# Kernel tuning notes

Hardware: AMD Instinct MI355X
Metric: run time of the kernel (lower is better)

Reference implementation:

```python
import jax, jax.numpy as jnp
import numpy as np

VOL = 128
FACTOR = 0.5 * VOL
N = 262144
LAT = 16
B = 8


def setup_inputs() -> dict:
    key = jax.random.key(0)
    ks = jax.random.split(key, 10)
    x = jax.random.normal(ks[0], (B, LAT), jnp.float32)
    inds = jax.random.randint(ks[1], (N, 3), 1, 126, dtype=jnp.int32)
    reference_values = jax.random.normal(ks[2], (N,), jnp.float32)
    # SIREN first layer: U(-1/in, 1/in)
    W0 = jax.random.uniform(ks[3], (LAT, 8), jnp.float32, -1.0 / LAT, 1.0 / LAT)
    b0 = jnp.zeros((8,), jnp.float32)
    # SIREN hidden layers (4 residual layers): U(-sqrt(6/in), sqrt(6/in))
    lim_h = float(np.sqrt(6.0 / 8.0))
    Wh = jax.random.uniform(ks[4], (4, 8, 8), jnp.float32, -lim_h, lim_h)
    bh = jnp.zeros((4, 8), jnp.float32)
    # final glorot-uniform layer: 8 -> 4N
    lim_f = float(np.sqrt(6.0 / (8.0 + 4.0 * N)))
    Wf = jax.random.uniform(ks[5], (8, 4 * N), jnp.float32, -lim_f, lim_f)
    bf = jnp.zeros((4 * N,), jnp.float32)
    return {"x": x, "W0": W0, "b0": b0, "Wh": Wh, "bh": bh, "Wf": Wf,
            "bf": bf, "reference_values": reference_values, "inds": inds}


def _siren_mlp(x, W0, b0, Wh, bh, Wf, bf):
    bf16 = jnp.bfloat16
    h = jnp.sin(30.0 * (x.astype(bf16) @ W0.astype(bf16) + b0.astype(bf16)))
    for i in range(Wh.shape[0]):  # 4 residual sine layers, 8-wide
        h = h + jnp.sin(h @ Wh[i].astype(bf16) + bh[i].astype(bf16))
    return h.astype(jnp.float32) @ Wf + bf  # [B, 4N], final layer in fp32


def reference(x, W0, b0, Wh, bh, Wf, bf, reference_values, inds):
    Bn = x.shape[0]
    out = _siren_mlp(x, W0, b0, Wh, bh, Wf, bf).reshape(Bn, N, 4)
    delta_coords, delta_values = out[..., :3], out[..., 3]
    # coords = stack(z,y,x reversed) normalized to [-1,1)
    coords_norm = (jnp.stack([inds[:, 2], inds[:, 1], inds[:, 0]], axis=1)
                   .astype(jnp.float32) - FACTOR) / FACTOR  # [N,3]
    values = reference_values + delta_values                 # [B,N]
    coords = FACTOR * (coords_norm[None] + delta_coords) + FACTOR  # [B,N,3]
    bposf = jnp.floor(coords)
    bposi = bposf.astype(jnp.int32)
    f = coords - bposf
    fx, fy, fz = f[..., 0], f[..., 1], f[..., 2]
    gx, gy, gz = 1.0 - fx, 1.0 - fy, 1.0 - fz
    # 8 trilinear weights, in the original concat order
    w = jnp.stack([gx * gy * gz, fx * gy * gz, gx * fy * gz, gx * gy * fz,
                   gx * fy * fz, fx * gy * fz, fx * fy * gz, fx * fy * fz],
                  axis=1)                                    # [B,8,N]
    bamp = (values[:, None, :] * w).reshape(Bn, 8 * N)
    offs = jnp.array([[0, 0, 0], [1, 0, 0], [0, 1, 0], [0, 0, 1],
                      [0, 1, 1], [1, 0, 1], [1, 1, 0], [1, 1, 1]], jnp.int32)
    bpos = (bposi[:, None, :, :] + offs[None, :, None, :]).reshape(Bn, 8 * N, 3)

    def scatter(pos, amp):
        return jnp.zeros((VOL, VOL, VOL), jnp.float32).at[
            pos[:, 2], pos[:, 1], pos[:, 0]].add(amp)

    grids = jax.vmap(scatter)(bpos, bamp)  # [B,128,128,128]
    return grids
```

## Files before the change

### kernel.cpp

```cpp
#include <hip/hip_runtime.h>
#include <math.h>

#define VOL   128
#define V2    (VOL*VOL)
#define V3    (VOL*VOL*VOL)
#define NPTS  262144
#define LATD  16
#define BATCH 8
#define FACTORF 64.0f
#define NBINS (VOL*VOL)
#define RZ 8
#define RY 8
#define NREG 256
#define FAR_CAP 8192

#define WS_HBUF    0u
#define WS_HIST    256u
#define WS_START   65792u
#define WS_CURSOR  131584u
#define WS_RANK    197120u
#define WS_KEYS    1245696u
#define WS_FARCNT  2294272u
#define WS_FARLIST 2294528u
#define WS_COORDS  2327296u
#define WS_FULL    35881728u

__device__ __forceinline__ float bf16r(float x) {
    unsigned u = __float_as_uint(x);
    u = (u + 0x7fffu + ((u >> 16) & 1u)) & 0xffff0000u;
    return __uint_as_float(u);
}

__global__ void mlp_kernel(const float* __restrict__ x,
                           const float* __restrict__ W0,
                           const float* __restrict__ b0,
                           const float* __restrict__ Wh,
                           const float* __restrict__ bh,
                           float* __restrict__ hout) {
    int b = threadIdx.x;
    if (b >= BATCH) return;
    float xb[LATD];
    #pragma unroll
    for (int i = 0; i < LATD; ++i) xb[i] = bf16r(x[b*LATD + i]);
    float h[8];
    #pragma unroll
    for (int j = 0; j < 8; ++j) {
        float acc = 0.f;
        #pragma unroll
        for (int i = 0; i < LATD; ++i) acc += xb[i] * bf16r(W0[i*8 + j]);
        float t = bf16r(acc);
        t = bf16r(t + bf16r(b0[j]));
        t = bf16r(30.0f * t);
        h[j] = bf16r(sinf(t));
    }
    for (int l = 0; l < 4; ++l) {
        float nh[8];
        #pragma unroll
        for (int j = 0; j < 8; ++j) {
            float acc = 0.f;
            #pragma unroll
            for (int r = 0; r < 8; ++r) acc += h[r] * bf16r(Wh[(l*8 + r)*8 + j]);
            float t = bf16r(acc);
            t = bf16r(t + bf16r(bh[l*8 + j]));
            float s = bf16r(sinf(t));
            nh[j] = bf16r(h[j] + s);
        }
        #pragma unroll
        for (int j = 0; j < 8; ++j) h[j] = nh[j];
    }
    #pragma unroll
    for (int j = 0; j < 8; ++j) hout[b*8 + j] = h[j];
}

__global__ __launch_bounds__(256) void hist_kernel(const int* __restrict__ inds,
                                                   unsigned* __restrict__ hist) {
    int n = blockIdx.x * 256 + threadIdx.x;
    if (n >= NPTS) return;
    atomicAdd(&hist[inds[n*3]*VOL + inds[n*3+1]], 1u);
}

__global__ __launch_bounds__(256) void scan_kernel(const unsigned* __restrict__ hist,
                                                   unsigned* __restrict__ binstart,
                                                   unsigned* __restrict__ cursor) {
    __shared__ unsigned part[256];
    int t = threadIdx.x;
    const int CH = NBINS / 256;
    unsigned s = 0;
    for (int k = 0; k < CH; ++k) s += hist[t*CH + k];
    part[t] = s; __syncthreads();
    for (int off = 1; off < 256; off <<= 1) {
        unsigned v = (t >= off) ? part[t - off] : 0u;
        __syncthreads();
        part[t] += v;
        __syncthreads();
    }
    unsigned run = (t == 0) ? 0u : part[t - 1];
    for (int k = 0; k < CH; ++k) {
        int idx = t*CH + k;
        binstart[idx] = run;
        cursor[idx]   = run;
        run += hist[idx];
    }
    if (t == 255) binstart[NBINS] = NPTS;
}

__global__ __launch_bounds__(256) void rank_kernel(const int* __restrict__ inds,
                                                   unsigned* __restrict__ cursor,
                                                   unsigned* __restrict__ rank) {
    int n = blockIdx.x * 256 + threadIdx.x;
    if (n >= NPTS) return;
    rank[n] = atomicAdd(&cursor[inds[n*3]*VOL + inds[n*3+1]], 1u);
}

__global__ __launch_bounds__(256) void coords_kernel(
    const float* __restrict__ Wf, const float* __restrict__ bfv_g,
    const float* __restrict__ rv, const int* __restrict__ inds,
    const float* __restrict__ hbuf, const unsigned* __restrict__ rank,
    float4* __restrict__ coords_s, unsigned* __restrict__ keys)
{
    __shared__ float hs[64];
    if (threadIdx.x < 64) hs[threadIdx.x] = hbuf[threadIdx.x];
    __syncthreads();
    int n = blockIdx.x * 256 + threadIdx.x;
    if (n >= NPTS) return;
    int iz = inds[n*3], iy = inds[n*3+1], ix = inds[n*3+2];
    float cnx = ((float)ix - FACTORF) / FACTORF;
    float cny = ((float)iy - FACTORF) / FACTORF;
    float cnz = ((float)iz - FACTORF) / FACTORF;
    float val0 = rv[n];
    float4 bfv = ((const float4*)bfv_g)[n];
    float4 wf[8];
    #pragma unroll
    for (int r = 0; r < 8; ++r)
        wf[r] = ((const float4*)(Wf + (size_t)r * 4 * NPTS))[n];
    unsigned pos = rank[n];
    keys[pos] = (unsigned)((iz << 7) | iy);
    #pragma unroll
    for (int b = 0; b < BATCH; ++b) {
        float o0 = bfv.x, o1 = bfv.y, o2 = bfv.z, o3 = bfv.w;
        #pragma unroll
        for (int r = 0; r < 8; ++r) {
            float hv = hs[b*8 + r];
            o0 = fmaf(hv, wf[r].x, o0);
            o1 = fmaf(hv, wf[r].y, o1);
            o2 = fmaf(hv, wf[r].z, o2);
            o3 = fmaf(hv, wf[r].w, o3);
        }
        float4 c;
        c.x = FACTORF * (cnx + o0) + FACTORF;
        c.y = FACTORF * (cny + o1) + FACTORF;
        c.z = FACTORF * (cnz + o2) + FACTORF;
        c.w = val0 + o3;
        coords_s[(size_t)b * NPTS + pos] = c;
    }
}

__global__ __launch_bounds__(256) void region_kernel(
    const float4* __restrict__ coords_s, const unsigned* __restrict__ keys,
    const unsigned* __restrict__ binstart,
    unsigned* __restrict__ farcnt, unsigned* __restrict__ farlist,
    float* __restrict__ out)
{
    __shared__ float tile[RZ*RY*VOL];
    int tid = threadIdx.x;
    int b   = blockIdx.x >> 8;
    int rid = blockIdx.x & 255;
    int z0 = (rid >> 4) * RZ, y0 = (rid & 15) * RY;
    for (int i = tid; i < RZ*RY*VOL; i += 256) tile[i] = 0.f;
    __syncthreads();

    int ylo = y0 - 3, yhi = y0 + RY + 2;
    int sA0, sA1, sB0, sB1;
    if (ylo < 0)        { sA0 = ylo + VOL; sA1 = VOL; sB0 = 0; sB1 = yhi; }
    else if (yhi > VOL) { sA0 = ylo; sA1 = VOL; sB0 = 0; sB1 = yhi - VOL; }
    else                { sA0 = ylo; sA1 = yhi; sB0 = 0; sB1 = 0; }

    const float4* cb = coords_s + (size_t)b * NPTS;
    const int ox[8] = {0,1,0,0,0,1,1,1};
    const int oy[8] = {0,0,1,0,1,0,1,1};
    const int oz[8] = {0,0,0,1,1,1,0,1};

    for (int zr = z0 - 3; zr < z0 + RZ + 2; ++zr) {
        int zz = (zr + VOL) & (VOL-1);
        int base = zz * VOL;
        for (int sg = 0; sg < 2; ++sg) {
            int a  = sg ? sB0 : sA0;
            int e2 = sg ? sB1 : sA1;
            if (a >= e2) continue;
            unsigned s = binstart[base + a];
            unsigned e = binstart[base + e2];
            for (unsigned i = s + tid; i < e; i += 256) {
                unsigned kv = keys[i];
                int piz = kv >> 7, piy = kv & 127;
                float4 c = cb[i];
                float fxf = floorf(c.x), fyf = floorf(c.y), fzf = floorf(c.z);
                int bx = (int)fxf, by = (int)fyf, bz = (int)fzf;
                bool near = ((unsigned)(bz - piz + 2) <= 4u) &&
                            ((unsigned)(by - piy + 2) <= 4u);
                if (near) {
                    float fx = c.x - fxf, fy = c.y - fyf, fz = c.z - fzf;
                    float gx = 1.f - fx, gy = 1.f - fy, gz = 1.f - fz;
                    float val = c.w;
                    float w[8] = {gx*gy*gz, fx*gy*gz, gx*fy*gz, gx*gy*fz,
                                  gx*fy*fz, fx*gy*fz, fx*fy*gz, fx*fy*fz};
                    #pragma unroll
                    for (int o = 0; o < 8; ++o) {
                        int Z = (bz + oz[o]) & 127;
                        int Y = (by + oy[o]) & 127;
                        int X = (bx + ox[o]) & 127;
                        int dz = Z - z0, dy = Y - y0;
                        if ((unsigned)dz < RZ && (unsigned)dy < RY)
                            atomicAdd(&tile[(dz << 10) + (dy << 7) + X], val * w[o]);
                    }
                } else if (piz >= z0 && piz < z0+RZ && piy >= y0 && piy < y0+RY) {
                    unsigned pos = atomicAdd(farcnt, 1u);
                    if (pos < FAR_CAP) farlist[pos] = (i << 3) | (unsigned)b;
                }
            }
        }
    }
    __syncthreads();
    size_t ob = (size_t)b * V3;
    for (int i = tid; i < RZ*RY*VOL; i += 256) {
        int lz = i >> 10, rem = i & 1023, ly = rem >> 7, lx = rem & 127;
        out[ob + (size_t)(z0+lz)*V2 + (y0+ly)*VOL + lx] = tile[i];
    }
}

__global__ __launch_bounds__(256) void far_kernel(
    const float4* __restrict__ coords_s,
    const unsigned* __restrict__ farcnt, const unsigned* __restrict__ farlist,
    float* __restrict__ out)
{
    unsigned cnt = *farcnt;
    if (cnt > FAR_CAP) cnt = FAR_CAP;
    const int ox[8] = {0,1,0,0,0,1,1,1};
    const int oy[8] = {0,0,1,0,1,0,1,1};
    const int oz[8] = {0,0,0,1,1,1,0,1};
    for (unsigned idx = blockIdx.x * 256 + threadIdx.x; idx < cnt;
         idx += gridDim.x * 256) {
        unsigned e = farlist[idx];
        unsigned pid = e >> 3;
        int b = (int)(e & 7u);
        float4 c = coords_s[(size_t)b * NPTS + pid];
        float fxf = floorf(c.x), fyf = floorf(c.y), fzf = floorf(c.z);
        int bx = (int)fxf, by = (int)fyf, bz = (int)fzf;
        float fx = c.x - fxf, fy = c.y - fyf, fz = c.z - fzf;
        float gx = 1.f - fx, gy = 1.f - fy, gz = 1.f - fz;
        float val = c.w;
        float w[8] = {gx*gy*gz, fx*gy*gz, gx*fy*gz, gx*gy*fz,
                      gx*fy*fz, fx*gy*fz, fx*fy*gz, fx*fy*fz};
        float* ob = out + (size_t)b * V3;
        #pragma unroll
        for (int o = 0; o < 8; ++o) {
            int Z = (bz + oz[o]) & 127;
            int Y = (by + oy[o]) & 127;
            int X = (bx + ox[o]) & 127;
            atomicAdd(ob + (size_t)Z*V2 + Y*VOL + X, val * w[o]);
        }
    }
}

__global__ __launch_bounds__(256) void scatter_fallback(
    const float* __restrict__ Wf, const float* __restrict__ bfv_g,
    const float* __restrict__ rv, const int* __restrict__ inds,
    const float* __restrict__ hbuf, float* __restrict__ out)
{
    __shared__ float hs[BATCH*8];
    if (threadIdx.x < BATCH*8) hs[threadIdx.x] = hbuf[threadIdx.x];
    __syncthreads();
    int n = blockIdx.x * blockDim.x + threadIdx.x;
    if (n >= NPTS) return;
    int iz = inds[n*3 + 0], iy = inds[n*3 + 1], ix = inds[n*3 + 2];
    float cnx = ((float)ix - FACTORF) / FACTORF;
    float cny = ((float)iy - FACTORF) / FACTORF;
    float cnz = ((float)iz - FACTORF) / FACTORF;
    float val0 = rv[n];
    float4 bfv = ((const float4*)bfv_g)[n];
    float4 wf[8];
    #pragma unroll
    for (int r = 0; r < 8; ++r)
        wf[r] = ((const float4*)(Wf + (size_t)r * 4 * NPTS))[n];
    static const int offs[8][3] = {{0,0,0},{1,0,0},{0,1,0},{0,0,1},
                                   {0,1,1},{1,0,1},{1,1,0},{1,1,1}};
    #pragma unroll
    for (int b = 0; b < BATCH; ++b) {
        float o0 = bfv.x, o1 = bfv.y, o2 = bfv.z, o3 = bfv.w;
        #pragma unroll
        for (int r = 0; r < 8; ++r) {
            float hv = hs[b*8 + r];
            o0 = fmaf(hv, wf[r].x, o0);
            o1 = fmaf(hv, wf[r].y, o1);
            o2 = fmaf(hv, wf[r].z, o2);
            o3 = fmaf(hv, wf[r].w, o3);
        }
        float cx = FACTORF * (cnx + o0) + FACTORF;
        float cy = FACTORF * (cny + o1) + FACTORF;
        float cz = FACTORF * (cnz + o2) + FACTORF;
        float val = val0 + o3;
        float fxf = floorf(cx), fyf = floorf(cy), fzf = floorf(cz);
        int bx = (int)fxf, by = (int)fyf, bz = (int)fzf;
        float fx = cx - fxf, fy = cy - fyf, fz = cz - fzf;
        float gx = 1.f - fx, gy = 1.f - fy, gz = 1.f - fz;
        float w[8] = {gx*gy*gz, fx*gy*gz, gx*fy*gz, gx*gy*fz,
                      gx*fy*fz, fx*gy*fz, fx*fy*gz, fx*fy*fz};
        float* ob = out + (size_t)b * V3;
        #pragma unroll
        for (int o = 0; o < 8; ++o) {
            int X = (bx + offs[o][0]) & (VOL-1);
            int Y = (by + offs[o][1]) & (VOL-1);
            int Z = (bz + offs[o][2]) & (VOL-1);
            atomicAdd(ob + (size_t)Z*V2 + Y*VOL + X, val * w[o]);
        }
    }
}

extern "C" void kernel_launch(void* const* d_in, const int* in_sizes, int n_in,
                              void* d_out, int out_size, void* d_ws, size_t ws_size,
                              hipStream_t stream) {
    const float* x    = (const float*)d_in[0];
    const float* W0   = (const float*)d_in[1];
    const float* b0   = (const float*)d_in[2];
    const float* Wh   = (const float*)d_in[3];
    const float* bh   = (const float*)d_in[4];
    const float* Wf   = (const float*)d_in[5];
    const float* bf   = (const float*)d_in[6];
    const float* rv   = (const float*)d_in[7];
    const int*   inds = (const int*)d_in[8];
    float* out = (float*)d_out;
    char*  ws  = (char*)d_ws;

    float*    hbuf     = (float*)(ws + WS_HBUF);
    unsigned* hist     = (unsigned*)(ws + WS_HIST);
    unsigned* binstart = (unsigned*)(ws + WS_START);
    unsigned* cursor   = (unsigned*)(ws + WS_CURSOR);
    unsigned* rank     = (unsigned*)(ws + WS_RANK);
    unsigned* keys     = (unsigned*)(ws + WS_KEYS);
    unsigned* farcnt   = (unsigned*)(ws + WS_FARCNT);
    unsigned* farlist  = (unsigned*)(ws + WS_FARLIST);
    float4*   coords_s = (float4*)(ws + WS_COORDS);

    mlp_kernel<<<1, 64, 0, stream>>>(x, W0, b0, Wh, bh, hbuf);

    if (ws_size >= (size_t)WS_FULL) {
        hipMemsetAsync(hist, 0, NBINS*4, stream);
        hipMemsetAsync(farcnt, 0, 4, stream);
        hist_kernel<<<NPTS/256, 256, 0, stream>>>(inds, hist);
        scan_kernel<<<1, 256, 0, stream>>>(hist, binstart, cursor);
        rank_kernel<<<NPTS/256, 256, 0, stream>>>(inds, cursor, rank);
        coords_kernel<<<NPTS/256, 256, 0, stream>>>(Wf, bf, rv, inds, hbuf,
                                                    rank, coords_s, keys);
        region_kernel<<<NREG*BATCH, 256, 0, stream>>>(coords_s, keys, binstart,
                                                      farcnt, farlist, out);
        far_kernel<<<8, 256, 0, stream>>>(coords_s, farcnt, farlist, out);
    } else {
        hipMemsetAsync(d_out, 0, (size_t)out_size * sizeof(float), stream);
        scatter_fallback<<<NPTS/256, 256, 0, stream>>>(Wf, bf, rv, inds, hbuf, out);
    }
}
```

Baseline: 194.5 us.

## Fuse hist/rank, move far detection to coords, persistent region workers

Merges the histogram and rank passes into one atomic pass, with each point's rank taken relative to its bin start, which removes the cursor array and one kernel launch. Far-point detection moves into coords_kernel so every point is classified once, rather than inside every region block. Keys shrink to 16-bit. The region kernel becomes a persistent grid of 1280 workgroups that pull regions from an atomic counter, trading a global atomic per region for better load balance and lower launch overhead.

```diff
diff --git a/kernel.cpp b/kernel.cpp
--- a/kernel.cpp
+++ b/kernel.cpp
@@ -11,19 +11,19 @@
 #define NBINS (VOL*VOL)
 #define RZ 8
 #define RY 8
-#define NREG 256
+#define NREG_TOTAL 2048
+#define REGION_WGS 1280
 #define FAR_CAP 8192
 
 #define WS_HBUF    0u
 #define WS_HIST    256u
 #define WS_START   65792u
-#define WS_CURSOR  131584u
-#define WS_RANK    197120u
-#define WS_KEYS    1245696u
-#define WS_FARCNT  2294272u
-#define WS_FARLIST 2294528u
-#define WS_COORDS  2327296u
-#define WS_FULL    35881728u
+#define WS_RANK    131344u
+#define WS_KEYS    1179920u
+#define WS_CTRL    1704208u
+#define WS_FARLIST 1704240u
+#define WS_COORDS  1737008u
+#define WS_FULL    35291440u
 
 __device__ __forceinline__ float bf16r(float x) {
     unsigned u = __float_as_uint(x);
@@ -72,16 +72,17 @@
     for (int j = 0; j < 8; ++j) hout[b*8 + j] = h[j];
 }
 
-__global__ __launch_bounds__(256) void hist_kernel(const int* __restrict__ inds,
-                                                   unsigned* __restrict__ hist) {
+__global__ __launch_bounds__(256) void hist_rank_kernel(const int* __restrict__ inds,
+                                                        unsigned* __restrict__ hist,
+                                                        unsigned* __restrict__ rank) {
     int n = blockIdx.x * 256 + threadIdx.x;
     if (n >= NPTS) return;
-    atomicAdd(&hist[inds[n*3]*VOL + inds[n*3+1]], 1u);
+    rank[n] = atomicAdd(&hist[inds[n*3]*VOL + inds[n*3+1]], 1u);
 }
 
 __global__ __launch_bounds__(256) void scan_kernel(const unsigned* __restrict__ hist,
                                                    unsigned* __restrict__ binstart,
-                                                   unsigned* __restrict__ cursor) {
+                                                   unsigned* __restrict__ ctrl) {
     __shared__ unsigned part[256];
     int t = threadIdx.x;
     const int CH = NBINS / 256;
@@ -98,25 +99,18 @@
     for (int k = 0; k < CH; ++k) {
         int idx = t*CH + k;
         binstart[idx] = run;
-        cursor[idx]   = run;
         run += hist[idx];
     }
-    if (t == 255) binstart[NBINS] = NPTS;
-}
-
-__global__ __launch_bounds__(256) void rank_kernel(const int* __restrict__ inds,
-                                                   unsigned* __restrict__ cursor,
-                                                   unsigned* __restrict__ rank) {
-    int n = blockIdx.x * 256 + threadIdx.x;
-    if (n >= NPTS) return;
-    rank[n] = atomicAdd(&cursor[inds[n*3]*VOL + inds[n*3+1]], 1u);
+    if (t == 0) { binstart[NBINS] = NPTS; ctrl[0] = 0u; ctrl[1] = 0u; }
 }
 
 __global__ __launch_bounds__(256) void coords_kernel(
     const float* __restrict__ Wf, const float* __restrict__ bfv_g,
     const float* __restrict__ rv, const int* __restrict__ inds,
-    const float* __restrict__ hbuf, const unsigned* __restrict__ rank,
-    float4* __restrict__ coords_s, unsigned* __restrict__ keys)
+    const float* __restrict__ hbuf, const unsigned* __restrict__ binstart,
+    const unsigned* __restrict__ rank, unsigned short* __restrict__ keys,
+    unsigned* __restrict__ ctrl, unsigned* __restrict__ farlist,
+    float4* __restrict__ coords_s)
 {
     __shared__ float hs[64];
     if (threadIdx.x < 64) hs[threadIdx.x] = hbuf[threadIdx.x];
@@ -133,8 +127,8 @@
     #pragma unroll
     for (int r = 0; r < 8; ++r)
         wf[r] = ((const float4*)(Wf + (size_t)r * 4 * NPTS))[n];
-    unsigned pos = rank[n];
-    keys[pos] = (unsigned)((iz << 7) | iy);
+    unsigned pos = binstart[iz*VOL + iy] + rank[n];
+    keys[pos] = (unsigned short)((iz << 7) | iy);
     #pragma unroll
     for (int b = 0; b < BATCH; ++b) {
         float o0 = bfv.x, o1 = bfv.y, o2 = bfv.z, o3 = bfv.w;
@@ -152,52 +146,68 @@
         c.z = FACTORF * (cnz + o2) + FACTORF;
         c.w = val0 + o3;
         coords_s[(size_t)b * NPTS + pos] = c;
+        int bz = (int)floorf(c.z), by = (int)floorf(c.y);
+        bool nearzy = ((unsigned)(bz - iz + 2) <= 4u) &&
+                      ((unsigned)(by - iy + 2) <= 4u);
+        if (!nearzy) {
+            unsigned fp = atomicAdd(&ctrl[0], 1u);
+            if (fp < FAR_CAP) farlist[fp] = (pos << 3) | (unsigned)b;
+        }
     }
 }
 
 __global__ __launch_bounds__(256) void region_kernel(
-    const float4* __restrict__ coords_s, const unsigned* __restrict__ keys,
-    const unsigned* __restrict__ binstart,
-    unsigned* __restrict__ farcnt, unsigned* __restrict__ farlist,
+    const float4* __restrict__ coords_s, const unsigned short* __restrict__ keys,
+    const unsigned* __restrict__ binstart, unsigned* __restrict__ ctrl,
     float* __restrict__ out)
 {
     __shared__ float tile[RZ*RY*VOL];
+    __shared__ int reg_s;
     int tid = threadIdx.x;
-    int b   = blockIdx.x >> 8;
-    int rid = blockIdx.x & 255;
-    int z0 = (rid >> 4) * RZ, y0 = (rid & 15) * RY;
-    for (int i = tid; i < RZ*RY*VOL; i += 256) tile[i] = 0.f;
-    __syncthreads();
-
-    int ylo = y0 - 3, yhi = y0 + RY + 2;
-    int sA0, sA1, sB0, sB1;
-    if (ylo < 0)        { sA0 = ylo + VOL; sA1 = VOL; sB0 = 0; sB1 = yhi; }
-    else if (yhi > VOL) { sA0 = ylo; sA1 = VOL; sB0 = 0; sB1 = yhi - VOL; }
-    else                { sA0 = ylo; sA1 = yhi; sB0 = 0; sB1 = 0; }
-
-    const float4* cb = coords_s + (size_t)b * NPTS;
+
     const int ox[8] = {0,1,0,0,0,1,1,1};
     const int oy[8] = {0,0,1,0,1,0,1,1};
     const int oz[8] = {0,0,0,1,1,1,0,1};
 
-    for (int zr = z0 - 3; zr < z0 + RZ + 2; ++zr) {
-        int zz = (zr + VOL) & (VOL-1);
-        int base = zz * VOL;
-        for (int sg = 0; sg < 2; ++sg) {
-            int a  = sg ? sB0 : sA0;
-            int e2 = sg ? sB1 : sA1;
-            if (a >= e2) continue;
-            unsigned s = binstart[base + a];
-            unsigned e = binstart[base + e2];
-            for (unsigned i = s + tid; i < e; i += 256) {
-                unsigned kv = keys[i];
-                int piz = kv >> 7, piy = kv & 127;
-                float4 c = cb[i];
-                float fxf = floorf(c.x), fyf = floorf(c.y), fzf = floorf(c.z);
-                int bx = (int)fxf, by = (int)fyf, bz = (int)fzf;
-                bool near = ((unsigned)(bz - piz + 2) <= 4u) &&
-                            ((unsigned)(by - piy + 2) <= 4u);
-                if (near) {
+    for (;;) {
+        __syncthreads();
+        if (tid == 0) reg_s = (int)atomicAdd(&ctrl[1], 1u);
+        __syncthreads();
+        int reg = reg_s;
+        if (reg >= NREG_TOTAL) return;
+        int b   = reg >> 8;
+        int rid = reg & 255;
+        int z0 = (rid >> 4) * RZ, y0 = (rid & 15) * RY;
+
+        for (int i = tid; i < RZ*RY*VOL; i += 256) tile[i] = 0.f;
+        __syncthreads();
+
+        int ylo = y0 - 3, yhi = y0 + RY + 2;
+        int sA0, sA1, sB0, sB1;
+        if (ylo < 0)        { sA0 = ylo + VOL; sA1 = VOL; sB0 = 0; sB1 = yhi; }
+        else if (yhi > VOL) { sA0 = ylo; sA1 = VOL; sB0 = 0; sB1 = yhi - VOL; }
+        else                { sA0 = ylo; sA1 = yhi; sB0 = 0; sB1 = 0; }
+
+        const float4* cb = coords_s + (size_t)b * NPTS;
+
+        for (int zr = z0 - 3; zr < z0 + RZ + 2; ++zr) {
+            int zz = (zr + VOL) & (VOL-1);
+            int base = zz * VOL;
+            for (int sg = 0; sg < 2; ++sg) {
+                int a  = sg ? sB0 : sA0;
+                int e2 = sg ? sB1 : sA1;
+                if (a >= e2) continue;
+                unsigned s = binstart[base + a];
+                unsigned e = binstart[base + e2];
+                for (unsigned i = s + tid; i < e; i += 256) {
+                    unsigned kv = keys[i];
+                    int piz = (int)(kv >> 7), piy = (int)(kv & 127);
+                    float4 c = cb[i];
+                    float fxf = floorf(c.x), fyf = floorf(c.y), fzf = floorf(c.z);
+                    int bx = (int)fxf, by = (int)fyf, bz = (int)fzf;
+                    bool nearzy = ((unsigned)(bz - piz + 2) <= 4u) &&
+                                  ((unsigned)(by - piy + 2) <= 4u);
+                    if (!nearzy) continue;
                     float fx = c.x - fxf, fy = c.y - fyf, fz = c.z - fzf;
                     float gx = 1.f - fx, gy = 1.f - fy, gz = 1.f - fz;
                     float val = c.w;
@@ -205,34 +215,30 @@
                                   gx*fy*fz, fx*gy*fz, fx*fy*gz, fx*fy*fz};
                     #pragma unroll
                     for (int o = 0; o < 8; ++o) {
-                        int Z = (bz + oz[o]) & 127;
-                        int Y = (by + oy[o]) & 127;
+                        int Z = (bz + oz[o]) & 127, dz = Z - z0;
+                        if ((unsigned)dz >= RZ) continue;
+                        int Y = (by + oy[o]) & 127, dy = Y - y0;
+                        if ((unsigned)dy >= RY) continue;
                         int X = (bx + ox[o]) & 127;
-                        int dz = Z - z0, dy = Y - y0;
-                        if ((unsigned)dz < RZ && (unsigned)dy < RY)
-                            atomicAdd(&tile[(dz << 10) + (dy << 7) + X], val * w[o]);
+                        atomicAdd(&tile[(dz << 10) + (dy << 7) + X], val * w[o]);
                     }
-                } else if (piz >= z0 && piz < z0+RZ && piy >= y0 && piy < y0+RY) {
-                    unsigned pos = atomicAdd(farcnt, 1u);
-                    if (pos < FAR_CAP) farlist[pos] = (i << 3) | (unsigned)b;
                 }
             }
         }
-    }
-    __syncthreads();
-    size_t ob = (size_t)b * V3;
-    for (int i = tid; i < RZ*RY*VOL; i += 256) {
-        int lz = i >> 10, rem = i & 1023, ly = rem >> 7, lx = rem & 127;
-        out[ob + (size_t)(z0+lz)*V2 + (y0+ly)*VOL + lx] = tile[i];
+        __syncthreads();
+        size_t ob = (size_t)b * V3;
+        for (int i = tid; i < RZ*RY*VOL; i += 256) {
+            int lz = i >> 10, ly = (i >> 7) & (RY-1), lx = i & 127;
+            out[ob + (size_t)(z0+lz)*V2 + (y0+ly)*VOL + lx] = tile[i];
+        }
     }
 }
 
 __global__ __launch_bounds__(256) void far_kernel(
-    const float4* __restrict__ coords_s,
-    const unsigned* __restrict__ farcnt, const unsigned* __restrict__ farlist,
-    float* __restrict__ out)
+    const float4* __restrict__ coords_s, const unsigned* __restrict__ ctrl,
+    const unsigned* __restrict__ farlist, float* __restrict__ out)
 {
-    unsigned cnt = *farcnt;
+    unsigned cnt = ctrl[0];
     if (cnt > FAR_CAP) cnt = FAR_CAP;
     const int ox[8] = {0,1,0,0,0,1,1,1};
     const int oy[8] = {0,0,1,0,1,0,1,1};
@@ -240,9 +246,9 @@
     for (unsigned idx = blockIdx.x * 256 + threadIdx.x; idx < cnt;
          idx += gridDim.x * 256) {
         unsigned e = farlist[idx];
-        unsigned pid = e >> 3;
+        unsigned pos = e >> 3;
         int b = (int)(e & 7u);
-        float4 c = coords_s[(size_t)b * NPTS + pid];
+        float4 c = coords_s[(size_t)b * NPTS + pos];
         float fxf = floorf(c.x), fyf = floorf(c.y), fzf = floorf(c.z);
         int bx = (int)fxf, by = (int)fyf, bz = (int)fzf;
         float fx = c.x - fxf, fy = c.y - fyf, fz = c.z - fzf;
@@ -330,29 +336,27 @@
     float* out = (float*)d_out;
     char*  ws  = (char*)d_ws;
 
-    float*    hbuf     = (float*)(ws + WS_HBUF);
-    unsigned* hist     = (unsigned*)(ws + WS_HIST);
-    unsigned* binstart = (unsigned*)(ws + WS_START);
-    unsigned* cursor   = (unsigned*)(ws + WS_CURSOR);
-    unsigned* rank     = (unsigned*)(ws + WS_RANK);
-    unsigned* keys     = (unsigned*)(ws + WS_KEYS);
-    unsigned* farcnt   = (unsigned*)(ws + WS_FARCNT);
-    unsigned* farlist  = (unsigned*)(ws + WS_FARLIST);
-    float4*   coords_s = (float4*)(ws + WS_COORDS);
+    float*          hbuf     = (float*)(ws + WS_HBUF);
+    unsigned*       hist     = (unsigned*)(ws + WS_HIST);
+    unsigned*       binstart = (unsigned*)(ws + WS_START);
+    unsigned*       rank     = (unsigned*)(ws + WS_RANK);
+    unsigned short* keys     = (unsigned short*)(ws + WS_KEYS);
+    unsigned*       ctrl     = (unsigned*)(ws + WS_CTRL);
+    unsigned*       farlist  = (unsigned*)(ws + WS_FARLIST);
+    float4*         coords_s = (float4*)(ws + WS_COORDS);
 
     mlp_kernel<<<1, 64, 0, stream>>>(x, W0, b0, Wh, bh, hbuf);
 
     if (ws_size >= (size_t)WS_FULL) {
         hipMemsetAsync(hist, 0, NBINS*4, stream);
-        hipMemsetAsync(farcnt, 0, 4, stream);
-        hist_kernel<<<NPTS/256, 256, 0, stream>>>(inds, hist);
-        scan_kernel<<<1, 256, 0, stream>>>(hist, binstart, cursor);
-        rank_kernel<<<NPTS/256, 256, 0, stream>>>(inds, cursor, rank);
+        hist_rank_kernel<<<NPTS/256, 256, 0, stream>>>(inds, hist, rank);
+        scan_kernel<<<1, 256, 0, stream>>>(hist, binstart, ctrl);
         coords_kernel<<<NPTS/256, 256, 0, stream>>>(Wf, bf, rv, inds, hbuf,
-                                                    rank, coords_s, keys);
-        region_kernel<<<NREG*BATCH, 256, 0, stream>>>(coords_s, keys, binstart,
-                                                      farcnt, farlist, out);
-        far_kernel<<<8, 256, 0, stream>>>(coords_s, farcnt, farlist, out);
+                                                    binstart, rank, keys,
+                                                    ctrl, farlist, coords_s);
+        region_kernel<<<REGION_WGS, 256, 0, stream>>>(coords_s, keys, binstart,
+                                                      ctrl, out);
+        far_kernel<<<8, 256, 0, stream>>>(coords_s, ctrl, farlist, out);
     } else {
         hipMemsetAsync(d_out, 0, (size_t)out_size * sizeof(float), stream);
         scatter_fallback<<<NPTS/256, 256, 0, stream>>>(Wf, bf, rv, inds, hbuf, out);
```

New measurement: 200.8 us. 3.2% more time.
